# Kernel tuning notes

Measured on AMD Instinct MI355X. Metric: run time of the kernel, lower is better.

## Reference

```python
import jax, jax.numpy as jnp
import numpy as np

N = 100000      # nodes
E = 1250000     # edges
D = 64          # d_data
H = 256         # hidden dim
C = 40          # n_cls
K = 4           # propagation steps
ALPHA = 0.05
EPS = 1e-5      # BatchNorm eps


def setup_inputs() -> dict:
    key = jax.random.key(0)
    ks = jax.random.split(key, 8)
    feat = jax.random.normal(ks[0], (N, D), dtype=jnp.float32)
    src = jax.random.randint(ks[1], (E,), 0, N, dtype=jnp.int32)
    dst = jax.random.randint(ks[2], (E,), 0, N, dtype=jnp.int32)
    W1 = jax.random.normal(ks[3], (D, H), dtype=jnp.float32) * (1.0 / np.sqrt(D))
    W2 = jax.random.normal(ks[4], (H, H), dtype=jnp.float32) * (1.0 / np.sqrt(H))
    W3 = jax.random.normal(ks[5], (H, C), dtype=jnp.float32) * (1.0 / np.sqrt(H))
    return {
        "feat": feat, "src": src, "dst": dst,
        "W1": W1, "b1": jnp.zeros((H,), jnp.float32),
        "g1": jnp.ones((H,), jnp.float32), "be1": jnp.zeros((H,), jnp.float32),
        "W2": W2, "b2": jnp.zeros((H,), jnp.float32),
        "g2": jnp.ones((H,), jnp.float32), "be2": jnp.zeros((H,), jnp.float32),
        "W3": W3, "b3": jnp.zeros((C,), jnp.float32),
    }


def _batchnorm(x, gamma, beta):
    # BatchNorm1d in training mode: per-feature batch mean / biased var
    mu = jnp.mean(x, axis=0)
    var = jnp.var(x, axis=0)
    return gamma * (x - mu) * jax.lax.rsqrt(var + EPS) + beta


def reference(feat, src, dst, W1, b1, g1, be1, W2, b2, g2, be2, W3, b3):
    # --- S2GC aggregation: sum_{t=1..K} (D^-1/2 A D^-1/2)^t X ---
    deg = jax.ops.segment_sum(jnp.ones((E,), feat.dtype), dst, num_segments=N)
    norm = jnp.clip(deg, 1.0, None) ** -0.5          # [N]
    norm = norm[:, None]                              # [N,1]
    h = feat
    acc = jnp.zeros_like(feat)
    for _ in range(K):
        h = h * norm
        h = jax.ops.segment_sum(h[src], dst, num_segments=N)  # copy_u -> sum
        h = h * norm
        acc = acc + h
    x = (1.0 - ALPHA) / K * acc + ALPHA * feat
    # --- feat_trans MLP: (Linear -> BN -> ReLU) x2 -> Linear ---
    x = jax.nn.relu(_batchnorm(x @ W1 + b1, g1, be1))
    x = jax.nn.relu(_batchnorm(x @ W2 + b2, g2, be2))
    logits = x @ W3 + b3                              # mask is all-ones (tasks=None)
    return logits
```

## Files before the change

### kernel.cpp

```cpp
#include <hip/hip_runtime.h>

#define NN 100000
#define EE 1250000
#define DD 64
#define HH 256
#define NC_OUT 40
#define ALPHA_C 0.05f
#define COEF 0.2375f
#define EPS_C 1e-5f
#define NBUCK 391
#define EPB 8192
#define NB2 782
#define PART_ROWS (NB2 * 2)
#define NRED 16

typedef __attribute__((ext_vector_type(8))) short short8;
typedef __attribute__((ext_vector_type(4))) float f32x4;

static __device__ __forceinline__ float bf2f(unsigned int u) {
  union { float f; unsigned int i; } x; x.i = u << 16; return x.f;
}
static __device__ __forceinline__ unsigned short f2bf(float f) {
  unsigned int x = __float_as_uint(f);
  unsigned int r = (x + 0x7FFFu + ((x >> 16) & 1u)) >> 16;
  return (unsigned short)r;
}
static __device__ __forceinline__ float bfat(uint4 v, int j) {
  unsigned int u = ((const unsigned int*)&v)[j >> 1];
  return bf2f((j & 1) ? (u >> 16) : (u & 0xffffu));
}


__global__ void k_count(const int* __restrict__ dst, int* __restrict__ deg) {
  int e = blockIdx.x * 256 + threadIdx.x;
  if (e < EE) atomicAdd(&deg[dst[e]], 1);
}

__global__ void k_scan1(const int* __restrict__ deg, int* __restrict__ rp,
                        int* __restrict__ bsum) {
  __shared__ int ts[256];
  int t = threadIdx.x;
  int base = blockIdx.x * 2048 + t * 8;
  int v[8]; int s = 0;
#pragma unroll
  for (int l = 0; l < 8; l++) { int i = base + l; v[l] = (i < NN) ? deg[i] : 0; s += v[l]; }
  ts[t] = s; __syncthreads();
  for (int off = 1; off < 256; off <<= 1) {
    int x = (t >= off) ? ts[t - off] : 0;
    __syncthreads();
    ts[t] += x;
    __syncthreads();
  }
  int run = ts[t] - s;
#pragma unroll
  for (int l = 0; l < 8; l++) { int i = base + l; if (i < NN) rp[i] = run; run += v[l]; }
  if (t == 255) bsum[blockIdx.x] = ts[255];
}

__global__ void k_scan2(const int* __restrict__ bsum, int* __restrict__ boff, int nb) {
  __shared__ int ts[64];
  int t = threadIdx.x;
  int x = (t < nb) ? bsum[t] : 0;
  ts[t] = x; __syncthreads();
  for (int off = 1; off < 64; off <<= 1) {
    int y = (t >= off) ? ts[t - off] : 0;
    __syncthreads();
    ts[t] += y;
    __syncthreads();
  }
  boff[t] = ts[t] - x;
}

__global__ void k_scan3(int* __restrict__ rp, const int* __restrict__ boff,
                        const int* __restrict__ deg, float* __restrict__ norm,
                        float* __restrict__ rnorm, int* __restrict__ bcur) {
  int i = blockIdx.x * 256 + threadIdx.x;
  if (i < NN) {
    int r = rp[i] + boff[i >> 11];
    rp[i] = r;
    if ((i & 255) == 0) bcur[i >> 8] = r;
    int d = deg[i]; if (d < 1) d = 1;
    norm[i] = rsqrtf((float)d);
    rnorm[i] = sqrtf((float)d);
    if (i == 0) rp[NN] = EE;
  }
}

__global__ __launch_bounds__(256) void k_bucket(const int* __restrict__ src,
                                                const int* __restrict__ dst,
                                                int* __restrict__ bcur,
                                                unsigned int* __restrict__ pairbuf) {
  __shared__ int hist[NBUCK];
  __shared__ int gbase[NBUCK];
  __shared__ int lcur[NBUCK];
  int tid = threadIdx.x;
  int e0 = blockIdx.x * EPB;
  int e1 = e0 + EPB; if (e1 > EE) e1 = EE;
  for (int i = tid; i < NBUCK; i += 256) { hist[i] = 0; lcur[i] = 0; }
  __syncthreads();
  for (int e = e0 + tid; e < e1; e += 256) {
    int b = dst[e] >> 8;
    atomicAdd(&hist[b], 1);
  }
  __syncthreads();
  for (int b = tid; b < NBUCK; b += 256) {
    int h = hist[b];
    gbase[b] = h ? atomicAdd(&bcur[b], h) : 0;
  }
  __syncthreads();
  for (int e = e0 + tid; e < e1; e += 256) {
    int d = dst[e];
    int b = d >> 8;
    int r = atomicAdd(&lcur[b], 1);
    pairbuf[gbase[b] + r] = (unsigned int)src[e] | ((unsigned int)(d & 255) << 24);
  }
}

__global__ __launch_bounds__(256) void k_local(const unsigned int* __restrict__ pairbuf,
                                               const int* __restrict__ rp,
                                               int* __restrict__ srt) {
  __shared__ int cur[256];
  int b = blockIdx.x;
  int node0 = b << 8;
  int t = threadIdx.x;
  int node = node0 + t;
  cur[t] = (node < NN) ? rp[node] : 0;
  int lo = rp[node0];
  int hi = (node0 + 256 <= NN) ? rp[node0 + 256] : EE;
  __syncthreads();
  for (int e = lo + t; e < hi; e += 256) {
    unsigned int w = pairbuf[e];
    int s = (int)(w & 0x1FFFFu);
    int l = (int)(w >> 24);
    int p = atomicAdd(&cur[l], 1);
    srt[p] = s;
  }
}


__global__ void k_init(const float4* __restrict__ feat4, const float* __restrict__ norm,
                       uint2* __restrict__ hs) {
  int i = blockIdx.x * 256 + threadIdx.x;
  if (i < NN * 16) {
    float nv = norm[i >> 4];
    float4 f = feat4[i];
    uint2 o;
    o.x = (unsigned int)f2bf(f.x * nv) | ((unsigned int)f2bf(f.y * nv) << 16);
    o.y = (unsigned int)f2bf(f.z * nv) | ((unsigned int)f2bf(f.w * nv) << 16);
    hs[i] = o;
  }
}

__global__ void k_gather(const unsigned short* __restrict__ hin,
                         unsigned short* __restrict__ hout,
                         const int* __restrict__ rp,
                         const int* __restrict__ srt, const float* __restrict__ norm) {
  int node = blockIdx.x * 4 + (threadIdx.x >> 6);
  int lane = threadIdx.x & 63;
  if (node >= NN) return;
  int beg = rp[node], end = rp[node + 1];
  float s0 = 0.f, s1 = 0.f;
  int e = beg;
  for (; e + 8 <= end; e += 8) {
    int n0 = srt[e], n1 = srt[e + 1], n2 = srt[e + 2], n3 = srt[e + 3];
    int n4 = srt[e + 4], n5 = srt[e + 5], n6 = srt[e + 6], n7 = srt[e + 7];
    float x0 = bf2f(hin[(size_t)n0 * 64 + lane]);
    float x1 = bf2f(hin[(size_t)n1 * 64 + lane]);
    float x2 = bf2f(hin[(size_t)n2 * 64 + lane]);
    float x3 = bf2f(hin[(size_t)n3 * 64 + lane]);
    float x4 = bf2f(hin[(size_t)n4 * 64 + lane]);
    float x5 = bf2f(hin[(size_t)n5 * 64 + lane]);
    float x6 = bf2f(hin[(size_t)n6 * 64 + lane]);
    float x7 = bf2f(hin[(size_t)n7 * 64 + lane]);
    s0 += (x0 + x1) + (x2 + x3);
    s1 += (x4 + x5) + (x6 + x7);
  }
  if (e + 4 <= end) {
    int n0 = srt[e], n1 = srt[e + 1], n2 = srt[e + 2], n3 = srt[e + 3];
    float x0 = bf2f(hin[(size_t)n0 * 64 + lane]);
    float x1 = bf2f(hin[(size_t)n1 * 64 + lane]);
    float x2 = bf2f(hin[(size_t)n2 * 64 + lane]);
    float x3 = bf2f(hin[(size_t)n3 * 64 + lane]);
    s0 += (x0 + x1);
    s1 += (x2 + x3);
    e += 4;
  }
  if (e + 2 <= end) {
    int n0 = srt[e], n1 = srt[e + 1];
    s0 += bf2f(hin[(size_t)n0 * 64 + lane]);
    s1 += bf2f(hin[(size_t)n1 * 64 + lane]);
    e += 2;
  }
  if (e < end) s0 += bf2f(hin[(size_t)srt[e] * 64 + lane]);
  float nv = norm[node];
  hout[(size_t)node * 64 + lane] = f2bf((s0 + s1) * nv * nv);
}

__global__ void k_transWT(const float* __restrict__ W, unsigned short* __restrict__ BTt,
                          int K) {
  int col = blockIdx.x;
  int t = threadIdx.x;
  if (t >= (K >> 3)) return;
  int s = t >> 2, kg = t & 3;
  size_t o = (size_t)s * 8192 + (size_t)col * 32 + kg * 8;
#pragma unroll
  for (int j = 0; j < 8; j++)
    BTt[o + j] = f2bf(W[(size_t)(s * 32 + kg * 8 + j) * 256 + col]);
}

template <int KTOT, int MODE>
__global__ __launch_bounds__(512) void k_mfma(
    const unsigned short* __restrict__ h1, const unsigned short* __restrict__ h2,
    const unsigned short* __restrict__ h3, const unsigned short* __restrict__ h4,
    const float* __restrict__ feat, const float* __restrict__ rnorm,
    const unsigned short* __restrict__ Yin,
    const float* __restrict__ af, const float* __restrict__ cf,
    const unsigned short* __restrict__ BTt,
    unsigned short* __restrict__ Yout, float* __restrict__ part, int M) {
  constexpr int S = KTOT / 32;
  constexpr int LDA = 40;
  __shared__ unsigned short Al[128 * LDA];
  __shared__ float afl[256], cfl[256];
  const int tid = threadIdx.x;
  const int wid = tid >> 6, lane = tid & 63;
  const int rowg = wid >> 2, colg = wid & 3;
  const int rbase = blockIdx.x * 128;
  const int lr = lane & 15;
  const int kg = lane >> 4;
  const int r = tid >> 2;
  const int c8 = (tid & 3) * 8;
  int arow = rbase + r; if (arow >= M) arow = M - 1;

  if constexpr (MODE == 1) {
    if (tid < 256) { afl[tid] = af[tid]; cfl[tid] = cf[tid]; }
    __syncthreads();
  }

  f32x4 acc[4][4];
#pragma unroll
  for (int i = 0; i < 4; i++)
#pragma unroll
    for (int j = 0; j < 4; j++) acc[i][j] = (f32x4){0.f, 0.f, 0.f, 0.f};

  for (int s = 0; s < S; s++) {
    {
      float xv[8];
      if constexpr (MODE == 0) {
        size_t ho = (size_t)arow * 64 + s * 32 + c8;
        uint4 v1 = *(const uint4*)(h1 + ho);
        uint4 v2 = *(const uint4*)(h2 + ho);
        uint4 v3 = *(const uint4*)(h3 + ho);
        uint4 v4 = *(const uint4*)(h4 + ho);
        float rc = rnorm[arow] * COEF;
        const float* fp = feat + ho;
        float4 f0 = *(const float4*)fp, f1 = *(const float4*)(fp + 4);
        float ff[8] = { f0.x, f0.y, f0.z, f0.w, f1.x, f1.y, f1.z, f1.w };
#pragma unroll
        for (int j = 0; j < 8; j++) {
          float sm = (bfat(v1, j) + bfat(v2, j)) + (bfat(v3, j) + bfat(v4, j));
          xv[j] = rc * sm + ALPHA_C * ff[j];
        }
      } else {
        uint4 v = *(const uint4*)(Yin + (size_t)arow * 256 + s * 32 + c8);
        unsigned int u[4] = { v.x, v.y, v.z, v.w };
#pragma unroll
        for (int h = 0; h < 4; h++) {
          int kc = s * 32 + c8 + h * 2;
          xv[h * 2]     = fmaxf(fmaf(afl[kc],     bf2f(u[h] & 0xffffu), cfl[kc]),     0.f);
          xv[h * 2 + 1] = fmaxf(fmaf(afl[kc + 1], bf2f(u[h] >> 16),     cfl[kc + 1]), 0.f);
        }
      }
      uint4 pk;
      pk.x = (unsigned int)f2bf(xv[0]) | ((unsigned int)f2bf(xv[1]) << 16);
      pk.y = (unsigned int)f2bf(xv[2]) | ((unsigned int)f2bf(xv[3]) << 16);
      pk.z = (unsigned int)f2bf(xv[4]) | ((unsigned int)f2bf(xv[5]) << 16);
      pk.w = (unsigned int)f2bf(xv[6]) | ((unsigned int)f2bf(xv[7]) << 16);
      *(uint4*)&Al[r * LDA + c8] = pk;
    }
    __syncthreads();

    short8 bfrag[4];
#pragma unroll
    for (int ni = 0; ni < 4; ni++) {
      int col = colg * 64 + ni * 16 + lr;
      bfrag[ni] = *(const short8*)(BTt + (size_t)s * 8192 + (size_t)col * 32 + kg * 8);
    }
    short8 afrag[4];
#pragma unroll
    for (int mi = 0; mi < 4; mi++)
      afrag[mi] = *(const short8*)&Al[(rowg * 64 + mi * 16 + lr) * LDA + kg * 8];
#pragma unroll
    for (int mi = 0; mi < 4; mi++)
#pragma unroll
      for (int ni = 0; ni < 4; ni++)
        acc[mi][ni] = __builtin_amdgcn_mfma_f32_16x16x32_bf16(afrag[mi], bfrag[ni],
                                                              acc[mi][ni], 0, 0, 0);
    __syncthreads();
  }

#pragma unroll
  for (int mi = 0; mi < 4; mi++) {
#pragma unroll
    for (int reg = 0; reg < 4; reg++) {
      int row = rbase + rowg * 64 + mi * 16 + kg * 4 + reg;
      if (row < M) {
#pragma unroll
        for (int ni = 0; ni < 4; ni++) {
          int col = colg * 64 + ni * 16 + lr;
          Yout[(size_t)row * 256 + col] = f2bf(acc[mi][ni][reg]);
        }
      }
    }
  }

  float s4[4] = {0.f, 0.f, 0.f, 0.f};
  float q4[4] = {0.f, 0.f, 0.f, 0.f};
#pragma unroll
  for (int mi = 0; mi < 4; mi++) {
#pragma unroll
    for (int reg = 0; reg < 4; reg++) {
      int row = rbase + rowg * 64 + mi * 16 + kg * 4 + reg;
      if (row < M) {
#pragma unroll
        for (int ni = 0; ni < 4; ni++) {
          float v = acc[mi][ni][reg];
          s4[ni] += v;
          q4[ni] = fmaf(v, v, q4[ni]);
        }
      }
    }
  }
  float* pb = part + ((size_t)blockIdx.x * 2 + rowg) * 512;
#pragma unroll
  for (int ni = 0; ni < 4; ni++) {
    float s = s4[ni], q = q4[ni];
    s += __shfl_xor(s, 16); s += __shfl_xor(s, 32);
    q += __shfl_xor(q, 16); q += __shfl_xor(q, 32);
    if (kg == 0) {
      int col = colg * 64 + ni * 16 + lr;
      pb[col] = s;
      pb[256 + col] = q;
    }
  }
}

__global__ __launch_bounds__(512) void k_red(const float* __restrict__ part,
                                             float* __restrict__ red2) {
  int t = threadIdx.x;
  const int per = (PART_ROWS + NRED - 1) / NRED;
  int b0 = blockIdx.x * per;
  int b1 = b0 + per; if (b1 > PART_ROWS) b1 = PART_ROWS;
  float s = 0.f;
  for (int b = b0; b < b1; b++) s += part[(size_t)b * 512 + t];
  red2[(size_t)blockIdx.x * 512 + t] = s;
}

__global__ void k_fold(const float* __restrict__ red2,
                       const float* __restrict__ gam, const float* __restrict__ bet,
                       float* __restrict__ af, float* __restrict__ cfv) {
  int c = threadIdx.x;
  float s = 0.f, q = 0.f;
#pragma unroll
  for (int r = 0; r < NRED; r++) {
    s += red2[(size_t)r * 512 + c];
    q += red2[(size_t)r * 512 + 256 + c];
  }
  float m = s * (1.0f / NN);
  float var = q * (1.0f / NN) - m * m;
  float a = gam[c] * rsqrtf(var + EPS_C);
  af[c] = a;
  cfv[c] = bet[c] - m * a;
}

__global__ __launch_bounds__(256) void k_gemm3(
    const unsigned short* __restrict__ Y2, const float* __restrict__ af,
    const float* __restrict__ cfv, const float* __restrict__ W3,
    const float* __restrict__ b3, float* __restrict__ out, int M) {
  __shared__ float Al[256 * 33];
  __shared__ float Wl[256 * 40];
  __shared__ float afl[256], cfl[256];
  int tid = threadIdx.x;
#pragma unroll
  for (int l = 0; l < 40; l++) Wl[l * 256 + tid] = W3[l * 256 + tid];
  afl[tid] = af[tid]; cfl[tid] = cfv[tid];
  __syncthreads();
  int rbase = blockIdx.x * 256;
  int rg = tid >> 3;
  int cg = tid & 7;
  float acc[8][5];
#pragma unroll
  for (int i = 0; i < 8; i++)
#pragma unroll
    for (int j = 0; j < 5; j++) acc[i][j] = 0.f;

  for (int k0 = 0; k0 < 256; k0 += 32) {
    int row = rbase + tid; if (row >= M) row = M - 1;
    const uint4* p = (const uint4*)(Y2 + (size_t)row * 256 + k0);
    uint4 vv[4]; vv[0] = p[0]; vv[1] = p[1]; vv[2] = p[2]; vv[3] = p[3];
    float* ap = &Al[tid * 33];
#pragma unroll
    for (int q = 0; q < 4; q++) {
      unsigned int u[4] = { vv[q].x, vv[q].y, vv[q].z, vv[q].w };
#pragma unroll
      for (int h = 0; h < 4; h++) {
        int kc = k0 + q * 8 + h * 2;
        float x0 = bf2f(u[h] & 0xffffu);
        float x1 = bf2f(u[h] >> 16);
        x0 = fmaxf(fmaf(afl[kc], x0, cfl[kc]), 0.f);
        x1 = fmaxf(fmaf(afl[kc + 1], x1, cfl[kc + 1]), 0.f);
        ap[q * 8 + h * 2] = x0; ap[q * 8 + h * 2 + 1] = x1;
      }
    }
    __syncthreads();
#pragma unroll 4
    for (int kk = 0; kk < 32; kk++) {
      float b[5];
#pragma unroll
      for (int j = 0; j < 5; j++) b[j] = Wl[(k0 + kk) * 40 + cg * 5 + j];
#pragma unroll
      for (int i = 0; i < 8; i++) {
        float a = Al[(rg + 32 * i) * 33 + kk];
#pragma unroll
        for (int j = 0; j < 5; j++) acc[i][j] = fmaf(a, b[j], acc[i][j]);
      }
    }
    __syncthreads();
  }
#pragma unroll
  for (int i = 0; i < 8; i++) {
    int row = rbase + rg + 32 * i;
    if (row < M) {
#pragma unroll
      for (int j = 0; j < 5; j++)
        out[(size_t)row * 40 + cg * 5 + j] = acc[i][j] + b3[cg * 5 + j];
    }
  }
}


extern "C" void kernel_launch(void* const* d_in, const int* in_sizes, int n_in,
                              void* d_out, int out_size, void* d_ws, size_t ws_size,
                              hipStream_t stream) {
  const float* feat = (const float*)d_in[0];
  const int* src = (const int*)d_in[1];
  const int* dstv = (const int*)d_in[2];
  const float* W1 = (const float*)d_in[3];
  const float* g1 = (const float*)d_in[5];
  const float* be1 = (const float*)d_in[6];
  const float* W2 = (const float*)d_in[7];
  const float* g2 = (const float*)d_in[9];
  const float* be2 = (const float*)d_in[10];
  const float* W3 = (const float*)d_in[11];
  const float* b3 = (const float*)d_in[12];
  float* out = (float*)d_out;

  char* w = (char*)d_ws;
  size_t off = 0;
  auto alloc = [&](size_t bytes) -> char* {
    char* p = w + off;
    off = (off + bytes + 255) & ~(size_t)255;
    return p;
  };
  int* deg = (int*)alloc((size_t)NN * 4);
  int* rp = (int*)alloc((size_t)(NN + 1) * 4);
  int* bsum = (int*)alloc(256);
  int* boff = (int*)alloc(256);
  int* bcur = (int*)alloc((size_t)NBUCK * 4);
  float* norm = (float*)alloc((size_t)NN * 4);
  float* rnorm = (float*)alloc((size_t)NN * 4);
  int* srt = (int*)alloc((size_t)EE * 4);
  unsigned int* pairbuf = (unsigned int*)alloc((size_t)EE * 4);
  unsigned short* hs0 = (unsigned short*)alloc((size_t)NN * 64 * 2);
  unsigned short* hn1 = (unsigned short*)alloc((size_t)NN * 64 * 2);
  unsigned short* hn2 = (unsigned short*)alloc((size_t)NN * 64 * 2);
  unsigned short* hn3 = (unsigned short*)alloc((size_t)NN * 64 * 2);
  unsigned short* hn4 = (unsigned short*)alloc((size_t)NN * 64 * 2);
  unsigned short* Y1 = (unsigned short*)alloc((size_t)NN * 256 * 2);
  unsigned short* Y2 = (unsigned short*)alloc((size_t)NN * 256 * 2);
  unsigned short* W1T = (unsigned short*)alloc(256 * 64 * 2);
  unsigned short* W2T = (unsigned short*)alloc(256 * 256 * 2);
  float* part = (float*)alloc((size_t)PART_ROWS * 512 * 4);
  float* red2 = (float*)alloc((size_t)NRED * 512 * 4);
  float* a1 = (float*)alloc(256 * 4);
  float* c1 = (float*)alloc(256 * 4);
  float* a2 = (float*)alloc(256 * 4);
  float* c2 = (float*)alloc(256 * 4);

  hipMemsetAsync(deg, 0, (size_t)NN * 4, stream);

  const int EB = (EE + 255) / 256;
  const int NB = (NN + 255) / 256;
  const int SB = (NN + 2047) / 2048;
  const int BB = (EE + EPB - 1) / EPB;

  k_count<<<EB, 256, 0, stream>>>(dstv, deg);
  k_transWT<<<256, 64, 0, stream>>>(W1, W1T, 64);
  k_transWT<<<256, 64, 0, stream>>>(W2, W2T, 256);
  k_scan1<<<SB, 256, 0, stream>>>(deg, rp, bsum);
  k_scan2<<<1, 64, 0, stream>>>(bsum, boff, SB);
  k_scan3<<<NB, 256, 0, stream>>>(rp, boff, deg, norm, rnorm, bcur);
  k_bucket<<<BB, 256, 0, stream>>>(src, dstv, bcur, pairbuf);
  k_local<<<NBUCK, 256, 0, stream>>>(pairbuf, rp, srt);

  k_init<<<(NN * 16 + 255) / 256, 256, 0, stream>>>((const float4*)feat, norm, (uint2*)hs0);
  k_gather<<<(NN + 3) / 4, 256, 0, stream>>>(hs0, hn1, rp, srt, norm);
  k_gather<<<(NN + 3) / 4, 256, 0, stream>>>(hn1, hn2, rp, srt, norm);
  k_gather<<<(NN + 3) / 4, 256, 0, stream>>>(hn2, hn3, rp, srt, norm);
  k_gather<<<(NN + 3) / 4, 256, 0, stream>>>(hn3, hn4, rp, srt, norm);

  k_mfma<64, 0><<<NB2, 512, 0, stream>>>(hn1, hn2, hn3, hn4, feat, rnorm,
                                         nullptr, nullptr, nullptr, W1T, Y1, part, NN);
  k_red<<<NRED, 512, 0, stream>>>(part, red2);
  k_fold<<<1, 256, 0, stream>>>(red2, g1, be1, a1, c1);
  k_mfma<256, 1><<<NB2, 512, 0, stream>>>(nullptr, nullptr, nullptr, nullptr, nullptr,
                                          nullptr, Y1, a1, c1, W2T, Y2, part, NN);
  k_red<<<NRED, 512, 0, stream>>>(part, red2);
  k_fold<<<1, 256, 0, stream>>>(red2, g2, be2, a2, c2);
  k_gemm3<<<NB, 256, 0, stream>>>(Y2, a2, c2, W3, b3, out, NN);
}
```

Baseline: 562.1 us.

## Vectorize gather lanes across edges and move final GEMM to bf16 MFMA

The gather kernel now has each wavefront handle four edges at once. Each 16-lane group loads 8-byte chunks of a row, and the partial sums are combined with cross-lane shuffles. This replaces the previous one-bf16-per-lane loads and gives wider memory transactions and more edges in flight. The scalar fp32 final linear layer is replaced by an MFMA kernel that reads a transposed, padded bf16 copy of W3, so the output logits now come from a lower-precision bf16 matmul. The added shuffle reductions and idle lanes during the store are the cost of the gather change.

Measured after the change: 545.4 us. 3.0% less time.

```diff
diff --git a/kernel.cpp b/kernel.cpp
--- a/kernel.cpp
+++ b/kernel.cpp
@@ -151,49 +151,58 @@
   }
 }
 
-__global__ void k_gather(const unsigned short* __restrict__ hin,
-                         unsigned short* __restrict__ hout,
+__global__ void k_gather(const unsigned int* __restrict__ hin,
+                         unsigned int* __restrict__ hout,
                          const int* __restrict__ rp,
                          const int* __restrict__ srt, const float* __restrict__ norm) {
   int node = blockIdx.x * 4 + (threadIdx.x >> 6);
   int lane = threadIdx.x & 63;
   if (node >= NN) return;
   int beg = rp[node], end = rp[node + 1];
-  float s0 = 0.f, s1 = 0.f;
+  int g = lane >> 4;
+  int q = lane & 15;
+  float f0 = 0.f, f1 = 0.f, f2 = 0.f, f3 = 0.f;
   int e = beg;
   for (; e + 8 <= end; e += 8) {
-    int n0 = srt[e], n1 = srt[e + 1], n2 = srt[e + 2], n3 = srt[e + 3];
-    int n4 = srt[e + 4], n5 = srt[e + 5], n6 = srt[e + 6], n7 = srt[e + 7];
-    float x0 = bf2f(hin[(size_t)n0 * 64 + lane]);
-    float x1 = bf2f(hin[(size_t)n1 * 64 + lane]);
-    float x2 = bf2f(hin[(size_t)n2 * 64 + lane]);
-    float x3 = bf2f(hin[(size_t)n3 * 64 + lane]);
-    float x4 = bf2f(hin[(size_t)n4 * 64 + lane]);
-    float x5 = bf2f(hin[(size_t)n5 * 64 + lane]);
-    float x6 = bf2f(hin[(size_t)n6 * 64 + lane]);
-    float x7 = bf2f(hin[(size_t)n7 * 64 + lane]);
-    s0 += (x0 + x1) + (x2 + x3);
-    s1 += (x4 + x5) + (x6 + x7);
+    int nA = srt[e + g];
+    int nB = srt[e + 4 + g];
+    uint2 uA = *(const uint2*)&hin[(size_t)nA * 32 + q * 2];
+    uint2 uB = *(const uint2*)&hin[(size_t)nB * 32 + q * 2];
+    f0 += bf2f(uA.x & 0xffffu) + bf2f(uB.x & 0xffffu);
+    f1 += bf2f(uA.x >> 16)     + bf2f(uB.x >> 16);
+    f2 += bf2f(uA.y & 0xffffu) + bf2f(uB.y & 0xffffu);
+    f3 += bf2f(uA.y >> 16)     + bf2f(uB.y >> 16);
   }
   if (e + 4 <= end) {
-    int n0 = srt[e], n1 = srt[e + 1], n2 = srt[e + 2], n3 = srt[e + 3];
-    float x0 = bf2f(hin[(size_t)n0 * 64 + lane]);
-    float x1 = bf2f(hin[(size_t)n1 * 64 + lane]);
-    float x2 = bf2f(hin[(size_t)n2 * 64 + lane]);
-    float x3 = bf2f(hin[(size_t)n3 * 64 + lane]);
-    s0 += (x0 + x1);
-    s1 += (x2 + x3);
+    int nA = srt[e + g];
+    uint2 uA = *(const uint2*)&hin[(size_t)nA * 32 + q * 2];
+    f0 += bf2f(uA.x & 0xffffu);
+    f1 += bf2f(uA.x >> 16);
+    f2 += bf2f(uA.y & 0xffffu);
+    f3 += bf2f(uA.y >> 16);
     e += 4;
   }
-  if (e + 2 <= end) {
-    int n0 = srt[e], n1 = srt[e + 1];
-    s0 += bf2f(hin[(size_t)n0 * 64 + lane]);
-    s1 += bf2f(hin[(size_t)n1 * 64 + lane]);
-    e += 2;
-  }
-  if (e < end) s0 += bf2f(hin[(size_t)srt[e] * 64 + lane]);
-  float nv = norm[node];
-  hout[(size_t)node * 64 + lane] = f2bf((s0 + s1) * nv * nv);
+  int rem = end - e;
+  if (g < rem) {
+    int nA = srt[e + g];
+    uint2 uA = *(const uint2*)&hin[(size_t)nA * 32 + q * 2];
+    f0 += bf2f(uA.x & 0xffffu);
+    f1 += bf2f(uA.x >> 16);
+    f2 += bf2f(uA.y & 0xffffu);
+    f3 += bf2f(uA.y >> 16);
+  }
+  f0 += __shfl_xor(f0, 16); f0 += __shfl_xor(f0, 32);
+  f1 += __shfl_xor(f1, 16); f1 += __shfl_xor(f1, 32);
+  f2 += __shfl_xor(f2, 16); f2 += __shfl_xor(f2, 32);
+  f3 += __shfl_xor(f3, 16); f3 += __shfl_xor(f3, 32);
+  if (lane < 16) {
+    float nv = norm[node];
+    float nv2 = nv * nv;
+    uint2 o;
+    o.x = (unsigned int)f2bf(f0 * nv2) | ((unsigned int)f2bf(f1 * nv2) << 16);
+    o.y = (unsigned int)f2bf(f2 * nv2) | ((unsigned int)f2bf(f3 * nv2) << 16);
+    *(uint2*)&hout[(size_t)node * 32 + q * 2] = o;
+  }
 }
 
 __global__ void k_transWT(const float* __restrict__ W, unsigned short* __restrict__ BTt,
@@ -206,6 +215,16 @@
 #pragma unroll
   for (int j = 0; j < 8; j++)
     BTt[o + j] = f2bf(W[(size_t)(s * 32 + kg * 8 + j) * 256 + col]);
+}
+
+__global__ void k_transW3(const float* __restrict__ W3, unsigned short* __restrict__ BT3) {
+  int col = blockIdx.x;
+  int t = threadIdx.x;
+  int s = t >> 2, kg = t & 3;
+  size_t o = (size_t)s * 1536 + (size_t)col * 32 + kg * 8;
+#pragma unroll
+  for (int j = 0; j < 8; j++)
+    BT3[o + j] = (col < NC_OUT) ? f2bf(W3[(size_t)(s * 32 + kg * 8 + j) * NC_OUT + col]) : 0;
 }
 
 template <int KTOT, int MODE>
@@ -253,8 +272,8 @@
         uint4 v4 = *(const uint4*)(h4 + ho);
         float rc = rnorm[arow] * COEF;
         const float* fp = feat + ho;
-        float4 f0 = *(const float4*)fp, f1 = *(const float4*)(fp + 4);
-        float ff[8] = { f0.x, f0.y, f0.z, f0.w, f1.x, f1.y, f1.z, f1.w };
+        float4 f0 = *(const float4*)fp, f1v = *(const float4*)(fp + 4);
+        float ff[8] = { f0.x, f0.y, f0.z, f0.w, f1v.x, f1v.y, f1v.z, f1v.w };
 #pragma unroll
         for (int j = 0; j < 8; j++) {
           float sm = (bfat(v1, j) + bfat(v2, j)) + (bfat(v3, j) + bfat(v4, j));
@@ -344,6 +363,78 @@
   }
 }
 
+__global__ __launch_bounds__(512) void k_mfma3(
+    const unsigned short* __restrict__ Yin,
+    const float* __restrict__ af, const float* __restrict__ cf,
+    const unsigned short* __restrict__ BT3, const float* __restrict__ b3,
+    float* __restrict__ out, int M) {
+  constexpr int LDA = 40;
+  __shared__ unsigned short Al[128 * LDA];
+  __shared__ float afl[256], cfl[256], b3l[48];
+  const int tid = threadIdx.x;
+  const int wid = tid >> 6, lane = tid & 63;
+  const int rbase = blockIdx.x * 128;
+  const int lr = lane & 15;
+  const int kg = lane >> 4;
+  const int r = tid >> 2;
+  const int c8 = (tid & 3) * 8;
+  int arow = rbase + r; if (arow >= M) arow = M - 1;
+
+  if (tid < 256) { afl[tid] = af[tid]; cfl[tid] = cf[tid]; }
+  if (tid >= 256 && tid < 304) b3l[tid - 256] = (tid - 256 < NC_OUT) ? b3[tid - 256] : 0.f;
+  __syncthreads();
+
+  f32x4 acc[3];
+#pragma unroll
+  for (int j = 0; j < 3; j++) acc[j] = (f32x4){0.f, 0.f, 0.f, 0.f};
+
+  for (int s = 0; s < 8; s++) {
+    {
+      uint4 v = *(const uint4*)(Yin + (size_t)arow * 256 + s * 32 + c8);
+      unsigned int u[4] = { v.x, v.y, v.z, v.w };
+      float xv[8];
+#pragma unroll
+      for (int h = 0; h < 4; h++) {
+        int kc = s * 32 + c8 + h * 2;
+        xv[h * 2]     = fmaxf(fmaf(afl[kc],     bf2f(u[h] & 0xffffu), cfl[kc]),     0.f);
+        xv[h * 2 + 1] = fmaxf(fmaf(afl[kc + 1], bf2f(u[h] >> 16),     cfl[kc + 1]), 0.f);
+      }
+      uint4 pk;
+      pk.x = (unsigned int)f2bf(xv[0]) | ((unsigned int)f2bf(xv[1]) << 16);
+      pk.y = (unsigned int)f2bf(xv[2]) | ((unsigned int)f2bf(xv[3]) << 16);
+      pk.z = (unsigned int)f2bf(xv[4]) | ((unsigned int)f2bf(xv[5]) << 16);
+      pk.w = (unsigned int)f2bf(xv[6]) | ((unsigned int)f2bf(xv[7]) << 16);
+      *(uint4*)&Al[r * LDA + c8] = pk;
+    }
+    __syncthreads();
+
+    short8 bfrag[3];
+#pragma unroll
+    for (int ni = 0; ni < 3; ni++) {
+      int col = ni * 16 + lr;
+      bfrag[ni] = *(const short8*)(BT3 + (size_t)s * 1536 + (size_t)col * 32 + kg * 8);
+    }
+    short8 afrag = *(const short8*)&Al[(wid * 16 + lr) * LDA + kg * 8];
+#pragma unroll
+    for (int ni = 0; ni < 3; ni++)
+      acc[ni] = __builtin_amdgcn_mfma_f32_16x16x32_bf16(afrag, bfrag[ni], acc[ni], 0, 0, 0);
+    __syncthreads();
+  }
+
+#pragma unroll
+  for (int reg = 0; reg < 4; reg++) {
+    int row = rbase + wid * 16 + kg * 4 + reg;
+    if (row < M) {
+#pragma unroll
+      for (int ni = 0; ni < 3; ni++) {
+        int col = ni * 16 + lr;
+        if (col < NC_OUT)
+          out[(size_t)row * NC_OUT + col] = acc[ni][reg] + b3l[col];
+      }
+    }
+  }
+}
+
 __global__ __launch_bounds__(512) void k_red(const float* __restrict__ part,
                                              float* __restrict__ red2) {
   int t = threadIdx.x;
@@ -370,71 +461,6 @@
   float a = gam[c] * rsqrtf(var + EPS_C);
   af[c] = a;
   cfv[c] = bet[c] - m * a;
-}
-
-__global__ __launch_bounds__(256) void k_gemm3(
-    const unsigned short* __restrict__ Y2, const float* __restrict__ af,
-    const float* __restrict__ cfv, const float* __restrict__ W3,
-    const float* __restrict__ b3, float* __restrict__ out, int M) {
-  __shared__ float Al[256 * 33];
-  __shared__ float Wl[256 * 40];
-  __shared__ float afl[256], cfl[256];
-  int tid = threadIdx.x;
-#pragma unroll
-  for (int l = 0; l < 40; l++) Wl[l * 256 + tid] = W3[l * 256 + tid];
-  afl[tid] = af[tid]; cfl[tid] = cfv[tid];
-  __syncthreads();
-  int rbase = blockIdx.x * 256;
-  int rg = tid >> 3;
-  int cg = tid & 7;
-  float acc[8][5];
-#pragma unroll
-  for (int i = 0; i < 8; i++)
-#pragma unroll
-    for (int j = 0; j < 5; j++) acc[i][j] = 0.f;
-
-  for (int k0 = 0; k0 < 256; k0 += 32) {
-    int row = rbase + tid; if (row >= M) row = M - 1;
-    const uint4* p = (const uint4*)(Y2 + (size_t)row * 256 + k0);
-    uint4 vv[4]; vv[0] = p[0]; vv[1] = p[1]; vv[2] = p[2]; vv[3] = p[3];
-    float* ap = &Al[tid * 33];
-#pragma unroll
-    for (int q = 0; q < 4; q++) {
-      unsigned int u[4] = { vv[q].x, vv[q].y, vv[q].z, vv[q].w };
-#pragma unroll
-      for (int h = 0; h < 4; h++) {
-        int kc = k0 + q * 8 + h * 2;
-        float x0 = bf2f(u[h] & 0xffffu);
-        float x1 = bf2f(u[h] >> 16);
-        x0 = fmaxf(fmaf(afl[kc], x0, cfl[kc]), 0.f);
-        x1 = fmaxf(fmaf(afl[kc + 1], x1, cfl[kc + 1]), 0.f);
-        ap[q * 8 + h * 2] = x0; ap[q * 8 + h * 2 + 1] = x1;
-      }
-    }
-    __syncthreads();
-#pragma unroll 4
-    for (int kk = 0; kk < 32; kk++) {
-      float b[5];
-#pragma unroll
-      for (int j = 0; j < 5; j++) b[j] = Wl[(k0 + kk) * 40 + cg * 5 + j];
-#pragma unroll
-      for (int i = 0; i < 8; i++) {
-        float a = Al[(rg + 32 * i) * 33 + kk];
-#pragma unroll
-        for (int j = 0; j < 5; j++) acc[i][j] = fmaf(a, b[j], acc[i][j]);
-      }
-    }
-    __syncthreads();
-  }
-#pragma unroll
-  for (int i = 0; i < 8; i++) {
-    int row = rbase + rg + 32 * i;
-    if (row < M) {
-#pragma unroll
-      for (int j = 0; j < 5; j++)
-        out[(size_t)row * 40 + cg * 5 + j] = acc[i][j] + b3[cg * 5 + j];
-    }
-  }
 }
 
 
@@ -479,6 +505,7 @@
   unsigned short* Y2 = (unsigned short*)alloc((size_t)NN * 256 * 2);
   unsigned short* W1T = (unsigned short*)alloc(256 * 64 * 2);
   unsigned short* W2T = (unsigned short*)alloc(256 * 256 * 2);
+  unsigned short* W3T = (unsigned short*)alloc(48 * 256 * 2);
   float* part = (float*)alloc((size_t)PART_ROWS * 512 * 4);
   float* red2 = (float*)alloc((size_t)NRED * 512 * 4);
   float* a1 = (float*)alloc(256 * 4);
@@ -496,6 +523,7 @@
   k_count<<<EB, 256, 0, stream>>>(dstv, deg);
   k_transWT<<<256, 64, 0, stream>>>(W1, W1T, 64);
   k_transWT<<<256, 64, 0, stream>>>(W2, W2T, 256);
+  k_transW3<<<48, 32, 0, stream>>>(W3, W3T);
   k_scan1<<<SB, 256, 0, stream>>>(deg, rp, bsum);
   k_scan2<<<1, 64, 0, stream>>>(bsum, boff, SB);
   k_scan3<<<NB, 256, 0, stream>>>(rp, boff, deg, norm, rnorm, bcur);
@@ -503,10 +531,14 @@
   k_local<<<NBUCK, 256, 0, stream>>>(pairbuf, rp, srt);
 
   k_init<<<(NN * 16 + 255) / 256, 256, 0, stream>>>((const float4*)feat, norm, (uint2*)hs0);
-  k_gather<<<(NN + 3) / 4, 256, 0, stream>>>(hs0, hn1, rp, srt, norm);
-  k_gather<<<(NN + 3) / 4, 256, 0, stream>>>(hn1, hn2, rp, srt, norm);
-  k_gather<<<(NN + 3) / 4, 256, 0, stream>>>(hn2, hn3, rp, srt, norm);
-  k_gather<<<(NN + 3) / 4, 256, 0, stream>>>(hn3, hn4, rp, srt, norm);
+  k_gather<<<(NN + 3) / 4, 256, 0, stream>>>((const unsigned int*)hs0, (unsigned int*)hn1,
+                                             rp, srt, norm);
+  k_gather<<<(NN + 3) / 4, 256, 0, stream>>>((const unsigned int*)hn1, (unsigned int*)hn2,
+                                             rp, srt, norm);
+  k_gather<<<(NN + 3) / 4, 256, 0, stream>>>((const unsigned int*)hn2, (unsigned int*)hn3,
+                                             rp, srt, norm);
+  k_gather<<<(NN + 3) / 4, 256, 0, stream>>>((const unsigned int*)hn3, (unsigned int*)hn4,
+                                             rp, srt, norm);
 
   k_mfma<64, 0><<<NB2, 512, 0, stream>>>(hn1, hn2, hn3, hn4, feat, rnorm,
                                          nullptr, nullptr, nullptr, W1T, Y1, part, NN);
@@ -516,5 +548,5 @@
                                           nullptr, Y1, a1, c1, W2T, Y2, part, NN);
   k_red<<<NRED, 512, 0, stream>>>(part, red2);
   k_fold<<<1, 256, 0, stream>>>(red2, g2, be2, a2, c2);
-  k_gemm3<<<NB, 256, 0, stream>>>(Y2, a2, c2, W3, b3, out, NN);
-}
+  k_mfma3<<<NB2, 512, 0, stream>>>(Y2, a2, c2, W3T, b3, out, NN);
+}
```
